# Performance work log

Measured on AMD Instinct MI355X. Metric: run time of the kernel, lower is better.

## Reference

```python
import jax, jax.numpy as jnp
import numpy as np

N = 100000
E = 1600000
IN_C, HID_C, OUT_C = 128, 64, 64


def gcn_conv(x, W, b, src, dst, n_nodes):
    """PyG GCNConv: symmetric-normalized aggregation with self loops.
    out = D^{-1/2} (A + I) D^{-1/2} (x W) + b
    Self-loop contribution handled analytically instead of appending edges.
    """
    h = x @ W  # [N, out_c] transform first (smaller message dim)
    # degree including self loop
    deg = jnp.zeros((n_nodes,), dtype=x.dtype).at[dst].add(1.0) + 1.0
    dinv = jax.lax.rsqrt(deg)  # deg >= 1 due to self loops
    norm = dinv[src] * dinv[dst]  # [E]
    msg = h[src] * norm[:, None]  # [E, out_c] gather + scale
    agg = jnp.zeros_like(h).at[dst].add(msg)  # scatter-add
    agg = agg + h * (dinv * dinv)[:, None]  # self-loop term
    return agg + b


def setup_inputs() -> dict:
    key = jax.random.key(0)
    ks = jax.random.split(key, 8)
    x = jax.random.normal(ks[0], (N, IN_C), dtype=jnp.float32)
    edge_index = jax.random.randint(ks[1], (2, E), 0, N, dtype=jnp.int64)
    # Glorot-ish init scale for weights
    W1 = jax.random.normal(ks[2], (IN_C, HID_C), dtype=jnp.float32) * (1.0 / np.sqrt(IN_C))
    b1 = jnp.zeros((HID_C,), dtype=jnp.float32)
    W2 = jax.random.normal(ks[3], (HID_C, OUT_C), dtype=jnp.float32) * (1.0 / np.sqrt(HID_C))
    b2 = jnp.zeros((OUT_C,), dtype=jnp.float32)
    Wd = jax.random.normal(ks[4], (OUT_C, IN_C), dtype=jnp.float32) * (1.0 / np.sqrt(OUT_C))
    bd = jnp.zeros((IN_C,), dtype=jnp.float32)
    return {"x": x, "edge_index": edge_index, "W1": W1, "b1": b1,
            "W2": W2, "b2": b2, "Wd": Wd, "bd": bd}


def reference(x, edge_index, W1, b1, W2, b2, Wd, bd):
    src, dst = edge_index[0], edge_index[1]
    h = jax.nn.relu(gcn_conv(x, W1, b1, src, dst, N))
    z = gcn_conv(h, W2, b2, src, dst, N)
    x_hat = z @ Wd + bd  # dense decoder
    return x_hat
```

## Files before the change

### kernel.cpp

```cpp
#include <hip/hip_runtime.h>

constexpr int N_NODES = 100000;
constexpr int E_EDGES = 1600000;
constexpr int IN_C = 128, HID_C = 64, OUT_C = 64;
constexpr int IN_CP = 132;
constexpr int NPAD = 100096;
constexpr int DUMMY = N_NODES;
constexpr int BKT_SHIFT = 9;
constexpr int BKT_NODES = 512;
constexpr int NBKT = 196;
constexpr int CSR_CAP = 16384;
constexpr int CAPB = 16384;

__device__ __forceinline__ unsigned short f2bf(float f) {
    unsigned int u = __float_as_uint(f);
    unsigned int r = (u + 0x7FFFu + ((u >> 16) & 1u)) >> 16;
    return (unsigned short)r;
}
__device__ __forceinline__ float bflo(unsigned int u) {
    return __uint_as_float(u << 16);
}
__device__ __forceinline__ float bfhi(unsigned int u) {
    return __uint_as_float(u & 0xFFFF0000u);
}

__global__ void p0_zero(int* __restrict__ bcount,
                        unsigned short* __restrict__ g1, unsigned short* __restrict__ g2) {
    int t = threadIdx.x;
    if (t < NBKT) bcount[t] = 0;
    unsigned int* r1 = (unsigned int*)(g1 + (size_t)N_NODES * 64);
    unsigned int* r2 = (unsigned int*)(g2 + (size_t)N_NODES * 64);
    if (t < 64) { r1[t] = 0u; r2[t] = 0u; }
}

__global__ __launch_bounds__(256) void p1c_bin(const int* __restrict__ src,
                                               const int* __restrict__ dst,
                                               int* __restrict__ bcount,
                                               unsigned int* __restrict__ bbuf, int E) {
    __shared__ int lc[NBKT], lbase[NBKT];
    for (int i = threadIdx.x; i < NBKT; i += 256) lc[i] = 0;
    __syncthreads();
    int base = blockIdx.x * 4096;
    int s[16], d[16];
    for (int k = 0; k < 16; ++k) {
        int i = base + k * 256 + threadIdx.x;
        s[k] = (i < E) ? src[i] : -1;
        d[k] = (i < E) ? dst[i] : -1;
        if (d[k] >= 0) atomicAdd(&lc[d[k] >> BKT_SHIFT], 1);
    }
    __syncthreads();
    for (int i = threadIdx.x; i < NBKT; i += 256) {
        int c = lc[i];
        lbase[i] = c ? (i * CAPB + atomicAdd(&bcount[i], c)) : 0;
        lc[i] = 0;
    }
    __syncthreads();
    for (int k = 0; k < 16; ++k) {
        if (d[k] >= 0) {
            int b = d[k] >> BKT_SHIFT;
            int pos = lbase[b] + atomicAdd(&lc[b], 1);
            bbuf[pos] = (unsigned)s[k] | ((unsigned)(d[k] & (BKT_NODES - 1)) << 17);
        }
    }
}

__global__ __launch_bounds__(256) void p2_build(const unsigned int* __restrict__ bbuf,
                                                const int* __restrict__ bcount,
                                                int* __restrict__ csr,
                                                int* __restrict__ rowbeg,
                                                int* __restrict__ rowend,
                                                float* __restrict__ dinv) {
    __shared__ int cnt[BKT_NODES];
    __shared__ int beg[BKT_NODES];
    __shared__ int cur[BKT_NODES];
    __shared__ int tsum[256];
    int b = blockIdx.x;
    int t = threadIdx.x;
    int e0 = b * CAPB, ec = bcount[b];
    cnt[t] = 0; cnt[t + 256] = 0;
    __syncthreads();
    for (int i = t; i < ec; i += 256) {
        unsigned e = bbuf[e0 + i];
        atomicAdd(&cnt[e >> 17], 1);
    }
    __syncthreads();
    int c0 = cnt[2 * t], c1 = cnt[2 * t + 1];
    int a0 = (c0 + 7) & ~7;
    int a1 = (c1 + 7) & ~7;
    tsum[t] = a0 + a1;
    __syncthreads();
    for (int off = 1; off < 256; off <<= 1) {
        int v = (t >= off) ? tsum[t - off] : 0;
        __syncthreads();
        tsum[t] += v;
        __syncthreads();
    }
    int excl = tsum[t] - (a0 + a1);
    int gb = b * CSR_CAP;
    beg[2 * t] = excl;
    beg[2 * t + 1] = excl + a0;
    cur[2 * t] = 0; cur[2 * t + 1] = 0;
    int n0 = b * BKT_NODES + 2 * t;
    if (n0 < N_NODES) {
        rowbeg[n0] = gb + excl; rowend[n0] = gb + excl + a0;
        dinv[n0] = rsqrtf((float)c0 + 1.0f);
    }
    if (n0 + 1 < N_NODES) {
        rowbeg[n0 + 1] = gb + excl + a0; rowend[n0 + 1] = gb + excl + a0 + a1;
        dinv[n0 + 1] = rsqrtf((float)c1 + 1.0f);
    }
    __syncthreads();
    for (int i = t; i < ec; i += 256) {
        unsigned e = bbuf[e0 + i];
        int ln = e >> 17;
        int pos = beg[ln] + atomicAdd(&cur[ln], 1);
        csr[gb + pos] = (int)(e & 0x1FFFFu);
    }
    __syncthreads();
    {
        int p0 = beg[2 * t] + c0, p0e = beg[2 * t] + a0;
        for (int p = p0; p < p0e; ++p) csr[gb + p] = DUMMY;
        int p1 = beg[2 * t + 1] + c1, p1e = beg[2 * t + 1] + a1;
        for (int p = p1; p < p1e; ++p) csr[gb + p] = DUMMY;
    }
}

__device__ __forceinline__ void gather4(const unsigned short* __restrict__ g,
                                        const int* __restrict__ csr,
                                        int S, int e0, int e1, int e2, int e3, int lane,
                                        float2& A0, float2& A1, float2& A2, float2& A3) {
    const unsigned int* g32 = (const unsigned int*)g;
    int half = lane >> 5;
    int cp = lane & 31;
    float2 a0 = {0.f, 0.f}, a1 = {0.f, 0.f}, a2 = {0.f, 0.f}, a3 = {0.f, 0.f};
    for (int base = S; base < e3; base += 64) {
        int m = min(64, e3 - base);
        int sv = (lane < m) ? csr[base + lane] : 0;
        for (int j = 0; j < m; j += 8) {
            int p = base + j;
            int s0 = __shfl(sv, j + 0 + half);
            int s1 = __shfl(sv, j + 2 + half);
            int s2 = __shfl(sv, j + 4 + half);
            int s3 = __shfl(sv, j + 6 + half);
            unsigned u0 = g32[(size_t)s0 * 32 + cp];
            unsigned u1 = g32[(size_t)s1 * 32 + cp];
            unsigned u2 = g32[(size_t)s2 * 32 + cp];
            unsigned u3 = g32[(size_t)s3 * 32 + cp];
            float tx = (bflo(u0) + bflo(u1)) + (bflo(u2) + bflo(u3));
            float ty = (bfhi(u0) + bfhi(u1)) + (bfhi(u2) + bfhi(u3));
            if (p < e1) {
                if (p < e0) { a0.x += tx; a0.y += ty; } else { a1.x += tx; a1.y += ty; }
            } else {
                if (p < e2) { a2.x += tx; a2.y += ty; } else { a3.x += tx; a3.y += ty; }
            }
        }
    }
    a0.x += __shfl_xor(a0.x, 32); a0.y += __shfl_xor(a0.y, 32);
    a1.x += __shfl_xor(a1.x, 32); a1.y += __shfl_xor(a1.y, 32);
    a2.x += __shfl_xor(a2.x, 32); a2.y += __shfl_xor(a2.y, 32);
    a3.x += __shfl_xor(a3.x, 32); a3.y += __shfl_xor(a3.y, 32);
    A0 = a0; A1 = a1; A2 = a2; A3 = a3;
}

#define ROWOP(ACC, XR)                                                              \
    ACC[0] += XR.x * w0.x + XR.y * w1.x + XR.z * w2.x + XR.w * w3.x;                \
    ACC[1] += XR.x * w0.y + XR.y * w1.y + XR.z * w2.y + XR.w * w3.y;                \
    ACC[2] += XR.x * w0.z + XR.y * w1.z + XR.z * w2.z + XR.w * w3.z;                \
    ACC[3] += XR.x * w0.w + XR.y * w1.w + XR.z * w2.w + XR.w * w3.w;

__global__ __launch_bounds__(256) void gemm1_kernel(const float* __restrict__ x,
                                                    const float* __restrict__ W1,
                                                    const float* __restrict__ dinv,
                                                    unsigned short* __restrict__ g1) {
    __shared__ float xs[64][IN_CP];
    int n0 = blockIdx.x * 64;
    const float4* xv = (const float4*)(x + (size_t)n0 * IN_C);
    int maxv = (min(64, N_NODES - n0)) * (IN_C / 4);
    for (int i = threadIdx.x; i < 64 * (IN_C / 4); i += 256) {
        float4 v = (i < maxv) ? xv[i] : make_float4(0.f, 0.f, 0.f, 0.f);
        *(float4*)&xs[i >> 5][(i & 31) * 4] = v;
    }
    __syncthreads();
    int cg = (threadIdx.x & 15) * 4;
    int ng = (threadIdx.x >> 4) * 4;
    float acc0[4] = {0.f, 0.f, 0.f, 0.f};
    float acc1[4] = {0.f, 0.f, 0.f, 0.f};
    float acc2[4] = {0.f, 0.f, 0.f, 0.f};
    float acc3[4] = {0.f, 0.f, 0.f, 0.f};
#pragma unroll 4
    for (int k = 0; k < IN_C; k += 4) {
        float4 xr0 = *(const float4*)&xs[ng + 0][k];
        float4 xr1 = *(const float4*)&xs[ng + 1][k];
        float4 xr2 = *(const float4*)&xs[ng + 2][k];
        float4 xr3 = *(const float4*)&xs[ng + 3][k];
        float4 w0 = *(const float4*)&W1[(k + 0) * 64 + cg];
        float4 w1 = *(const float4*)&W1[(k + 1) * 64 + cg];
        float4 w2 = *(const float4*)&W1[(k + 2) * 64 + cg];
        float4 w3 = *(const float4*)&W1[(k + 3) * 64 + cg];
        ROWOP(acc0, xr0)
        ROWOP(acc1, xr1)
        ROWOP(acc2, xr2)
        ROWOP(acc3, xr3)
    }
#pragma unroll
    for (int i = 0; i < 4; ++i) {
        int n = n0 + ng + i;
        if (n < N_NODES) {
            float dv = dinv[n];
            const float* a = (i == 0) ? acc0 : (i == 1) ? acc1 : (i == 2) ? acc2 : acc3;
            ushort4 o;
            o.x = f2bf(a[0] * dv);
            o.y = f2bf(a[1] * dv);
            o.z = f2bf(a[2] * dv);
            o.w = f2bf(a[3] * dv);
            *(ushort4*)&g1[(size_t)n * 64 + cg] = o;
        }
    }
}

__global__ __launch_bounds__(256) void fused1_kernel(const unsigned short* __restrict__ g1,
                                                     const int* __restrict__ csr,
                                                     const int* __restrict__ rowbeg,
                                                     const int* __restrict__ rowend,
                                                     const float* __restrict__ dinv,
                                                     const float* __restrict__ b1,
                                                     const float* __restrict__ W2,
                                                     unsigned short* __restrict__ g2) {
    __shared__ float zs[16][64];
    int lane = threadIdx.x & 63;
    int w = threadIdx.x >> 6;
    int cp = lane & 31;
    int d0 = blockIdx.x * 16 + w * 4;
    int S  = __builtin_amdgcn_readfirstlane(rowbeg[d0]);
    int e0 = __builtin_amdgcn_readfirstlane(rowend[d0 + 0]);
    int e1 = __builtin_amdgcn_readfirstlane(rowend[d0 + 1]);
    int e2 = __builtin_amdgcn_readfirstlane(rowend[d0 + 2]);
    int e3 = __builtin_amdgcn_readfirstlane(rowend[d0 + 3]);
    float dv0 = dinv[d0 + 0], dv1 = dinv[d0 + 1], dv2 = dinv[d0 + 2], dv3 = dinv[d0 + 3];
    float2 a0, a1, a2, a3;
    gather4(g1, csr, S, e0, e1, e2, e3, lane, a0, a1, a2, a3);
    const unsigned int* g32 = (const unsigned int*)g1;
    unsigned su0 = g32[(size_t)(d0 + 0) * 32 + cp];
    unsigned su1 = g32[(size_t)(d0 + 1) * 32 + cp];
    unsigned su2 = g32[(size_t)(d0 + 2) * 32 + cp];
    unsigned su3 = g32[(size_t)(d0 + 3) * 32 + cp];
    float2 b1v = *(const float2*)&b1[2 * cp];
    int w4 = w * 4;
    if (lane < 32) {
        float2 z0 = make_float2(fmaxf(dv0 * (a0.x + bflo(su0)) + b1v.x, 0.f),
                                fmaxf(dv0 * (a0.y + bfhi(su0)) + b1v.y, 0.f));
        float2 z1 = make_float2(fmaxf(dv1 * (a1.x + bflo(su1)) + b1v.x, 0.f),
                                fmaxf(dv1 * (a1.y + bfhi(su1)) + b1v.y, 0.f));
        float2 z2 = make_float2(fmaxf(dv2 * (a2.x + bflo(su2)) + b1v.x, 0.f),
                                fmaxf(dv2 * (a2.y + bfhi(su2)) + b1v.y, 0.f));
        float2 z3 = make_float2(fmaxf(dv3 * (a3.x + bflo(su3)) + b1v.x, 0.f),
                                fmaxf(dv3 * (a3.y + bfhi(su3)) + b1v.y, 0.f));
        *(float2*)&zs[w4 + 0][2 * cp] = z0;
        *(float2*)&zs[w4 + 1][2 * cp] = z1;
        *(float2*)&zs[w4 + 2][2 * cp] = z2;
        *(float2*)&zs[w4 + 3][2 * cp] = z3;
    }
    float c0 = 0.f, c1 = 0.f, c2 = 0.f, c3 = 0.f;
#pragma unroll 8
    for (int k = 0; k < HID_C; ++k) {
        float wv = W2[k * 64 + lane];
        c0 += zs[w4 + 0][k] * wv;
        c1 += zs[w4 + 1][k] * wv;
        c2 += zs[w4 + 2][k] * wv;
        c3 += zs[w4 + 3][k] * wv;
    }
    g2[(size_t)(d0 + 0) * 64 + lane] = f2bf(dv0 * c0);
    g2[(size_t)(d0 + 1) * 64 + lane] = f2bf(dv1 * c1);
    g2[(size_t)(d0 + 2) * 64 + lane] = f2bf(dv2 * c2);
    g2[(size_t)(d0 + 3) * 64 + lane] = f2bf(dv3 * c3);
}

__global__ __launch_bounds__(256) void fused2_kernel(const unsigned short* __restrict__ g2,
                                                     const int* __restrict__ csr,
                                                     const int* __restrict__ rowbeg,
                                                     const int* __restrict__ rowend,
                                                     const float* __restrict__ dinv,
                                                     const float* __restrict__ b2,
                                                     const float* __restrict__ Wd,
                                                     const float* __restrict__ bd,
                                                     float* __restrict__ out) {
    __shared__ float zs[16][64];
    int lane = threadIdx.x & 63;
    int w = threadIdx.x >> 6;
    int cp = lane & 31;
    int d0 = blockIdx.x * 16 + w * 4;
    int S  = __builtin_amdgcn_readfirstlane(rowbeg[d0]);
    int e0 = __builtin_amdgcn_readfirstlane(rowend[d0 + 0]);
    int e1 = __builtin_amdgcn_readfirstlane(rowend[d0 + 1]);
    int e2 = __builtin_amdgcn_readfirstlane(rowend[d0 + 2]);
    int e3 = __builtin_amdgcn_readfirstlane(rowend[d0 + 3]);
    float dv0 = dinv[d0 + 0], dv1 = dinv[d0 + 1], dv2 = dinv[d0 + 2], dv3 = dinv[d0 + 3];
    float2 a0, a1, a2, a3;
    gather4(g2, csr, S, e0, e1, e2, e3, lane, a0, a1, a2, a3);
    const unsigned int* g32 = (const unsigned int*)g2;
    unsigned su0 = g32[(size_t)(d0 + 0) * 32 + cp];
    unsigned su1 = g32[(size_t)(d0 + 1) * 32 + cp];
    unsigned su2 = g32[(size_t)(d0 + 2) * 32 + cp];
    unsigned su3 = g32[(size_t)(d0 + 3) * 32 + cp];
    float2 b2v = *(const float2*)&b2[2 * cp];
    int w4 = w * 4;
    if (lane < 32) {
        float2 z0 = make_float2(dv0 * (a0.x + bflo(su0)) + b2v.x, dv0 * (a0.y + bfhi(su0)) + b2v.y);
        float2 z1 = make_float2(dv1 * (a1.x + bflo(su1)) + b2v.x, dv1 * (a1.y + bfhi(su1)) + b2v.y);
        float2 z2 = make_float2(dv2 * (a2.x + bflo(su2)) + b2v.x, dv2 * (a2.y + bfhi(su2)) + b2v.y);
        float2 z3 = make_float2(dv3 * (a3.x + bflo(su3)) + b2v.x, dv3 * (a3.y + bfhi(su3)) + b2v.y);
        *(float2*)&zs[w4 + 0][2 * cp] = z0;
        *(float2*)&zs[w4 + 1][2 * cp] = z1;
        *(float2*)&zs[w4 + 2][2 * cp] = z2;
        *(float2*)&zs[w4 + 3][2 * cp] = z3;
    }
    int cl = 2 * lane;
    float2 bdv = *(const float2*)&bd[cl];
    float c0x = bdv.x, c0y = bdv.y, c1x = bdv.x, c1y = bdv.y;
    float c2x = bdv.x, c2y = bdv.y, c3x = bdv.x, c3y = bdv.y;
    for (int k4 = 0; k4 < OUT_C; k4 += 4) {
        float4 z0 = *(const float4*)&zs[w4 + 0][k4];
        float4 z1 = *(const float4*)&zs[w4 + 1][k4];
        float4 z2 = *(const float4*)&zs[w4 + 2][k4];
        float4 z3 = *(const float4*)&zs[w4 + 3][k4];
#pragma unroll
        for (int kk = 0; kk < 4; ++kk) {
            float2 wv = *(const float2*)&Wd[(k4 + kk) * 128 + cl];
            float zz0 = ((const float*)&z0)[kk];
            float zz1 = ((const float*)&z1)[kk];
            float zz2 = ((const float*)&z2)[kk];
            float zz3 = ((const float*)&z3)[kk];
            c0x += zz0 * wv.x; c0y += zz0 * wv.y;
            c1x += zz1 * wv.x; c1y += zz1 * wv.y;
            c2x += zz2 * wv.x; c2y += zz2 * wv.y;
            c3x += zz3 * wv.x; c3y += zz3 * wv.y;
        }
    }
    *(float2*)&out[(size_t)(d0 + 0) * 128 + cl] = make_float2(c0x, c0y);
    *(float2*)&out[(size_t)(d0 + 1) * 128 + cl] = make_float2(c1x, c1y);
    *(float2*)&out[(size_t)(d0 + 2) * 128 + cl] = make_float2(c2x, c2y);
    *(float2*)&out[(size_t)(d0 + 3) * 128 + cl] = make_float2(c3x, c3y);
}

extern "C" void kernel_launch(void* const* d_in, const int* in_sizes, int n_in,
                              void* d_out, int out_size, void* d_ws, size_t ws_size,
                              hipStream_t stream) {
    const float* x = (const float*)d_in[0];
    const int* ei = (const int*)d_in[1];
    const int* src = ei;
    const int* dst = ei + E_EDGES;
    const float* W1 = (const float*)d_in[2];
    const float* b1 = (const float*)d_in[3];
    const float* W2 = (const float*)d_in[4];
    const float* b2 = (const float*)d_in[5];
    const float* Wd = (const float*)d_in[6];
    const float* bd = (const float*)d_in[7];
    float* out = (float*)d_out;

    int* bcount = (int*)d_ws;
    int* rowbeg = bcount + 256;
    int* rowend = rowbeg + NPAD;
    float* dinv = (float*)(rowend + NPAD);
    int* csr = (int*)(dinv + NPAD);
    unsigned short* g2 = (unsigned short*)(csr + NBKT * CSR_CAP);
    unsigned short* g1 = (unsigned short*)out;
    unsigned int* bbuf = (unsigned int*)((char*)d_out + 16000000);

    const int B = 256;
    const int EB = (E_EDGES + 4095) / 4096;

    p0_zero<<<1, B, 0, stream>>>(bcount, g1, g2);
    p1c_bin<<<EB, B, 0, stream>>>(src, dst, bcount, bbuf, E_EDGES);
    p2_build<<<NBKT, B, 0, stream>>>(bbuf, bcount, csr, rowbeg, rowend, dinv);

    gemm1_kernel<<<(N_NODES + 63) / 64, B, 0, stream>>>(x, W1, dinv, g1);
    fused1_kernel<<<N_NODES / 16, B, 0, stream>>>(g1, csr, rowbeg, rowend, dinv, b1, W2, g2);
    fused2_kernel<<<N_NODES / 16, B, 0, stream>>>(g2, csr, rowbeg, rowend, dinv, b2, Wd, bd, out);
}
```

Baseline: 213.2 us.

## Use bf16 MFMA for first-layer GEMM and split decoder column layout

The first-layer x@W1 GEMM now converts x and a transposed W1 to bf16 in shared memory and computes with 16x16x32 bf16 MFMA instructions instead of scalar fp32 FMAs. Every block re-transposes and converts W1, and bf16 inputs reduce precision relative to the fp32 reference. Separately, the decoder epilogue changes from float2 columns per lane to two scalar columns (lane and lane+64). The MFMA path writes output as scattered 2-byte stores per lane, which may coalesce worse.

```diff
diff --git a/kernel.cpp b/kernel.cpp
--- a/kernel.cpp
+++ b/kernel.cpp
@@ -3,7 +3,6 @@
 constexpr int N_NODES = 100000;
 constexpr int E_EDGES = 1600000;
 constexpr int IN_C = 128, HID_C = 64, OUT_C = 64;
-constexpr int IN_CP = 132;
 constexpr int NPAD = 100096;
 constexpr int DUMMY = N_NODES;
 constexpr int BKT_SHIFT = 9;
@@ -11,6 +10,9 @@
 constexpr int NBKT = 196;
 constexpr int CSR_CAP = 16384;
 constexpr int CAPB = 16384;
+
+typedef __attribute__((ext_vector_type(8))) short bf16x8;
+typedef __attribute__((ext_vector_type(4))) float f32x4;
 
 __device__ __forceinline__ unsigned short f2bf(float f) {
     unsigned int u = __float_as_uint(f);
@@ -162,58 +164,56 @@
     A0 = a0; A1 = a1; A2 = a2; A3 = a3;
 }
 
-#define ROWOP(ACC, XR)                                                              \
-    ACC[0] += XR.x * w0.x + XR.y * w1.x + XR.z * w2.x + XR.w * w3.x;                \
-    ACC[1] += XR.x * w0.y + XR.y * w1.y + XR.z * w2.y + XR.w * w3.y;                \
-    ACC[2] += XR.x * w0.z + XR.y * w1.z + XR.z * w2.z + XR.w * w3.z;                \
-    ACC[3] += XR.x * w0.w + XR.y * w1.w + XR.z * w2.w + XR.w * w3.w;
-
 __global__ __launch_bounds__(256) void gemm1_kernel(const float* __restrict__ x,
                                                     const float* __restrict__ W1,
                                                     const float* __restrict__ dinv,
                                                     unsigned short* __restrict__ g1) {
-    __shared__ float xs[64][IN_CP];
+    __shared__ unsigned short xsb[64 * 136];
+    __shared__ unsigned short wt[64 * 136];
+    int t = threadIdx.x;
     int n0 = blockIdx.x * 64;
     const float4* xv = (const float4*)(x + (size_t)n0 * IN_C);
-    int maxv = (min(64, N_NODES - n0)) * (IN_C / 4);
-    for (int i = threadIdx.x; i < 64 * (IN_C / 4); i += 256) {
+    int maxv = min(64, N_NODES - n0) * 32;
+    for (int i = t; i < 2048; i += 256) {
         float4 v = (i < maxv) ? xv[i] : make_float4(0.f, 0.f, 0.f, 0.f);
-        *(float4*)&xs[i >> 5][(i & 31) * 4] = v;
-    }
-    __syncthreads();
-    int cg = (threadIdx.x & 15) * 4;
-    int ng = (threadIdx.x >> 4) * 4;
-    float acc0[4] = {0.f, 0.f, 0.f, 0.f};
-    float acc1[4] = {0.f, 0.f, 0.f, 0.f};
-    float acc2[4] = {0.f, 0.f, 0.f, 0.f};
-    float acc3[4] = {0.f, 0.f, 0.f, 0.f};
-#pragma unroll 4
-    for (int k = 0; k < IN_C; k += 4) {
-        float4 xr0 = *(const float4*)&xs[ng + 0][k];
-        float4 xr1 = *(const float4*)&xs[ng + 1][k];
-        float4 xr2 = *(const float4*)&xs[ng + 2][k];
-        float4 xr3 = *(const float4*)&xs[ng + 3][k];
-        float4 w0 = *(const float4*)&W1[(k + 0) * 64 + cg];
-        float4 w1 = *(const float4*)&W1[(k + 1) * 64 + cg];
-        float4 w2 = *(const float4*)&W1[(k + 2) * 64 + cg];
-        float4 w3 = *(const float4*)&W1[(k + 3) * 64 + cg];
-        ROWOP(acc0, xr0)
-        ROWOP(acc1, xr1)
-        ROWOP(acc2, xr2)
-        ROWOP(acc3, xr3)
-    }
-#pragma unroll
-    for (int i = 0; i < 4; ++i) {
-        int n = n0 + ng + i;
-        if (n < N_NODES) {
-            float dv = dinv[n];
-            const float* a = (i == 0) ? acc0 : (i == 1) ? acc1 : (i == 2) ? acc2 : acc3;
-            ushort4 o;
-            o.x = f2bf(a[0] * dv);
-            o.y = f2bf(a[1] * dv);
-            o.z = f2bf(a[2] * dv);
-            o.w = f2bf(a[3] * dv);
-            *(ushort4*)&g1[(size_t)n * 64 + cg] = o;
+        int r = i >> 5, c4 = (i & 31) * 4;
+        ushort4 o;
+        o.x = f2bf(v.x); o.y = f2bf(v.y); o.z = f2bf(v.z); o.w = f2bf(v.w);
+        *(ushort4*)&xsb[r * 136 + c4] = o;
+    }
+    {
+        int c = t & 63, k0 = (t >> 6) * 32;
+        for (int kk = 0; kk < 32; ++kk)
+            wt[c * 136 + k0 + kk] = f2bf(W1[(k0 + kk) * 64 + c]);
+    }
+    __syncthreads();
+    int w = t >> 6, lane = t & 63;
+    int fr = lane & 15;
+    int ak = (lane >> 4) * 8;
+    int arow = w * 16 + fr;
+    bf16x8 afrag[4];
+#pragma unroll
+    for (int kc = 0; kc < 4; ++kc)
+        afrag[kc] = *(const bf16x8*)&xsb[arow * 136 + kc * 32 + ak];
+    f32x4 acc[4];
+#pragma unroll
+    for (int ni = 0; ni < 4; ++ni) acc[ni] = (f32x4){0.f, 0.f, 0.f, 0.f};
+#pragma unroll
+    for (int ni = 0; ni < 4; ++ni) {
+#pragma unroll
+        for (int kc = 0; kc < 4; ++kc) {
+            bf16x8 bfrag = *(const bf16x8*)&wt[(ni * 16 + fr) * 136 + kc * 32 + ak];
+            acc[ni] = __builtin_amdgcn_mfma_f32_16x16x32_bf16(afrag[kc], bfrag, acc[ni], 0, 0, 0);
+        }
+    }
+#pragma unroll
+    for (int j = 0; j < 4; ++j) {
+        int node = n0 + w * 16 + (lane >> 4) * 4 + j;
+        if (node < N_NODES) {
+            float dv = dinv[node];
+#pragma unroll
+            for (int ni = 0; ni < 4; ++ni)
+                g1[(size_t)node * 64 + ni * 16 + fr] = f2bf(acc[ni][j] * dv);
         }
     }
 }
@@ -314,10 +314,9 @@
         *(float2*)&zs[w4 + 2][2 * cp] = z2;
         *(float2*)&zs[w4 + 3][2 * cp] = z3;
     }
-    int cl = 2 * lane;
-    float2 bdv = *(const float2*)&bd[cl];
-    float c0x = bdv.x, c0y = bdv.y, c1x = bdv.x, c1y = bdv.y;
-    float c2x = bdv.x, c2y = bdv.y, c3x = bdv.x, c3y = bdv.y;
+    float bdl = bd[lane], bdh = bd[64 + lane];
+    float c0l = bdl, c0h = bdh, c1l = bdl, c1h = bdh;
+    float c2l = bdl, c2h = bdh, c3l = bdl, c3h = bdh;
     for (int k4 = 0; k4 < OUT_C; k4 += 4) {
         float4 z0 = *(const float4*)&zs[w4 + 0][k4];
         float4 z1 = *(const float4*)&zs[w4 + 1][k4];
@@ -325,21 +324,22 @@
         float4 z3 = *(const float4*)&zs[w4 + 3][k4];
 #pragma unroll
         for (int kk = 0; kk < 4; ++kk) {
-            float2 wv = *(const float2*)&Wd[(k4 + kk) * 128 + cl];
+            float w0 = Wd[(k4 + kk) * 128 + lane];
+            float w1 = Wd[(k4 + kk) * 128 + 64 + lane];
             float zz0 = ((const float*)&z0)[kk];
             float zz1 = ((const float*)&z1)[kk];
             float zz2 = ((const float*)&z2)[kk];
             float zz3 = ((const float*)&z3)[kk];
-            c0x += zz0 * wv.x; c0y += zz0 * wv.y;
-            c1x += zz1 * wv.x; c1y += zz1 * wv.y;
-            c2x += zz2 * wv.x; c2y += zz2 * wv.y;
-            c3x += zz3 * wv.x; c3y += zz3 * wv.y;
-        }
-    }
-    *(float2*)&out[(size_t)(d0 + 0) * 128 + cl] = make_float2(c0x, c0y);
-    *(float2*)&out[(size_t)(d0 + 1) * 128 + cl] = make_float2(c1x, c1y);
-    *(float2*)&out[(size_t)(d0 + 2) * 128 + cl] = make_float2(c2x, c2y);
-    *(float2*)&out[(size_t)(d0 + 3) * 128 + cl] = make_float2(c3x, c3y);
+            c0l += zz0 * w0; c0h += zz0 * w1;
+            c1l += zz1 * w0; c1h += zz1 * w1;
+            c2l += zz2 * w0; c2h += zz2 * w1;
+            c3l += zz3 * w0; c3h += zz3 * w1;
+        }
+    }
+    out[(size_t)(d0 + 0) * 128 + lane] = c0l; out[(size_t)(d0 + 0) * 128 + 64 + lane] = c0h;
+    out[(size_t)(d0 + 1) * 128 + lane] = c1l; out[(size_t)(d0 + 1) * 128 + 64 + lane] = c1h;
+    out[(size_t)(d0 + 2) * 128 + lane] = c2l; out[(size_t)(d0 + 2) * 128 + 64 + lane] = c2h;
+    out[(size_t)(d0 + 3) * 128 + lane] = c3l; out[(size_t)(d0 + 3) * 128 + 64 + lane] = c3h;
 }
 
 extern "C" void kernel_launch(void* const* d_in, const int* in_sizes, int n_in,
```

Result: faster. 173.4 us (median of 2 runs) (-18.7%).
